# Performance work log

Hardware: AMD Instinct MI355X
Metric: run time of the kernel (lower is better)

Reference implementation:

```python
import jax, jax.numpy as jnp
import numpy as np

D_MODEL = 1024
NUM_HEADS = 8
D_HEAD = D_MODEL // NUM_HEADS
EPS = 1e-5


def layer_norm(x, gamma, beta):
    mu = jnp.mean(x, axis=-1, keepdims=True)
    var = jnp.mean((x - mu) ** 2, axis=-1, keepdims=True)
    return (x - mu) * jax.lax.rsqrt(var + EPS) * gamma + beta


def setup_inputs() -> dict:
    key = jax.random.key(0)
    ks = jax.random.split(key, 16)
    B, N, M, D = 4, 1024, 1024, D_MODEL
    s = 0.02
    inp = {
        "input_states": jax.random.normal(ks[0], (B, N, D), jnp.float32),
        "memory_states": jax.random.normal(ks[1], (B, M, D), jnp.float32),
        "memory_weights": jax.random.uniform(ks[2], (B, M), jnp.float32),
        "memory_masks": jax.random.randint(ks[3], (B, M), 0, 2).astype(bool),
        "attention_factors": jax.random.uniform(ks[4], (B, N, M), jnp.float32),
        "attention_masks": jax.random.randint(ks[5], (B, 1, N, M), 0, 2).astype(bool),
        "Wq": jax.random.normal(ks[6], (D, D), jnp.float32) * s,
        "bq": jnp.zeros((D,), jnp.float32),
        "Wk": jax.random.normal(ks[7], (D, D), jnp.float32) * s,
        "bk": jnp.zeros((D,), jnp.float32),
        "Wv": jax.random.normal(ks[8], (D, D), jnp.float32) * s,
        "bv": jnp.zeros((D,), jnp.float32),
        "Wo": jax.random.normal(ks[9], (D, D), jnp.float32) * s,
        "bo": jnp.zeros((D,), jnp.float32),
        "g1": jnp.ones((D,), jnp.float32),
        "b1": jnp.zeros((D,), jnp.float32),
        "We": jax.random.normal(ks[10], (2 * D, D), jnp.float32) * s,
        "be": jnp.zeros((2 * D,), jnp.float32),
        "Ws": jax.random.normal(ks[11], (D, 2 * D), jnp.float32) * s,
        "bs": jnp.zeros((D,), jnp.float32),
        "g2": jnp.ones((D,), jnp.float32),
        "b2": jnp.zeros((D,), jnp.float32),
    }
    return inp


def reference(input_states, memory_states, memory_weights, memory_masks,
              attention_factors, attention_masks,
              Wq, bq, Wk, bk, Wv, bv, Wo, bo, g1, b1,
              We, be, Ws, bs, g2, b2):
    B, N, D = input_states.shape
    M = memory_states.shape[1]
    H, C = NUM_HEADS, D_HEAD
    # QKV projections, split heads: (B, H, len, C)
    q = (input_states @ Wq.T + bq).reshape(B, N, H, C).transpose(0, 2, 1, 3)
    k = (memory_states @ Wk.T + bk).reshape(B, M, H, C).transpose(0, 2, 1, 3)
    v = (memory_states @ Wv.T + bv).reshape(B, M, H, C).transpose(0, 2, 1, 3)
    scores = jnp.einsum('bhnc,bhmc->bhnm', q, k) / jnp.sqrt(jnp.float32(C))
    scores = attention_factors[:, None, :, :] * scores
    scores = scores * memory_weights[:, None, None, :]
    neg_inf = jnp.float32(-jnp.inf)
    scores = jnp.where(memory_masks[:, None, None, :], neg_inf, scores)
    scores = jnp.where(attention_masks, neg_inf, scores)
    attn = jax.nn.softmax(scores, axis=-1)  # (B,H,N,M)
    hidden = jnp.einsum('bhnm,bhmc->bhnc', attn, v)
    hidden = hidden.transpose(0, 2, 1, 3).reshape(B, N, D)
    hidden = hidden @ Wo.T + bo
    out1 = layer_norm(hidden + input_states, g1, b1)
    # FFN: expand -> ReLU -> squeeze -> residual + LN
    h = jax.nn.relu(out1 @ We.T + be)
    h = h @ Ws.T + bs
    out = layer_norm(out1 + h, g2, b2)
    return out, attn
```

## Files before the change

### kernel.cpp

```cpp
#include <hip/hip_runtime.h>
#include <hip/hip_bf16.h>

typedef __bf16 bf16_t;
typedef __bf16 bf16x4 __attribute__((ext_vector_type(4)));
typedef __bf16 bf16x8 __attribute__((ext_vector_type(8)));
typedef float f32x4 __attribute__((ext_vector_type(4)));

typedef const __attribute__((address_space(1))) void gvoid_t;
typedef __attribute__((address_space(3))) void lvoid_t;

#define MB (1UL<<20)
#define NEGINF (-__builtin_inff())
#define SCALE 0.08838834764831845f

__device__ __forceinline__ void gload_lds16(const void* g, void* l) {
    __builtin_amdgcn_global_load_lds((gvoid_t*)g, (lvoid_t*)l, 16, 0, 0);
}

__global__ __launch_bounds__(256)
void cast8_kernel(const float* __restrict__ s0, bf16_t* __restrict__ d0,
                  const float* __restrict__ s1, bf16_t* __restrict__ d1,
                  const float* __restrict__ s2, bf16_t* __restrict__ d2,
                  const float* __restrict__ s3, bf16_t* __restrict__ d3,
                  const float* __restrict__ s4, bf16_t* __restrict__ d4,
                  const float* __restrict__ s5, bf16_t* __restrict__ d5,
                  const float* __restrict__ s6, bf16_t* __restrict__ d6,
                  const float* __restrict__ s7, bf16_t* __restrict__ d7)
{
    long i = (long)blockIdx.x * 256 + threadIdx.x;
    const float* src; bf16_t* dst; long l;
    if      (i < 262144L)  { src = s0; dst = d0; l = i; }
    else if (i < 524288L)  { src = s1; dst = d1; l = i - 262144L; }
    else if (i < 786432L)  { src = s2; dst = d2; l = i - 524288L; }
    else if (i < 1048576L) { src = s3; dst = d3; l = i - 786432L; }
    else if (i < 1572864L) { src = s4; dst = d4; l = i - 1048576L; }
    else if (i < 2097152L) { src = s5; dst = d5; l = i - 1572864L; }
    else if (i < 3145728L) { src = s6; dst = d6; l = i - 2097152L; }
    else                   { src = s7; dst = d7; l = i - 3145728L; }
    float4 f = ((const float4*)src)[l];
    bf16x4 o;
    o[0] = (bf16_t)f.x; o[1] = (bf16_t)f.y; o[2] = (bf16_t)f.z; o[3] = (bf16_t)f.w;
    ((bf16x4*)dst)[l] = o;
}

template<int TM, int OUT_BF16, int HAS_BIAS, int RELU, int HAS_RES, int VT_OUT>
__global__ __launch_bounds__(256)
void gemm_bt(const bf16_t* __restrict__ Ap, int lda,
             const bf16_t* __restrict__ Bp, int ldb,
             const float* __restrict__ bias,
             const float* __restrict__ res, int ldres,
             void* __restrict__ Cp, int ldc,
             int K, int tilesN,
             long aOffB, long aOffH, long bOffB, long bOffH, long cOffZ, int nH)
{
    __shared__ bf16_t sA[2 * TM * 32];
    __shared__ bf16_t sB[2 * 128 * 32];

    const int z = blockIdx.y;
    const int zb = z / nH, zh = z % nH;
    Ap += zb * aOffB + zh * aOffH;
    Bp += zb * bOffB + zh * bOffH;
    const long cOff = (long)z * cOffZ;

    const int tile = blockIdx.x;
    const int tm = tile / tilesN, tn = tile % tilesN;
    const int rowBase = tm * TM, colBase = tn * 128;
    const int t = threadIdx.x;
    const int wave = t >> 6, lane = t & 63;
    const int wr = (TM == 128) ? ((wave >> 1) * 64) : 0;
    const int wc = (TM == 128) ? ((wave & 1) * 64) : (wave * 32);
    constexpr int NF = (TM == 128) ? 4 : 2;

    f32x4 acc[4][NF] = {};

    const int e0 = t * 8;
    const int srow = e0 >> 5, scol = e0 & 31;

    auto stage = [&](int tt, int bi) {
        const int k0 = tt * 32;
        #pragma unroll
        for (int r = 0; r < TM / 64; ++r) {
            const int row = r * 64 + srow;
            gload_lds16(Ap + (long)(rowBase + row) * lda + k0 + scol,
                        (char*)sA + bi * (TM * 64) + r * 4096 + wave * 1024);
        }
        #pragma unroll
        for (int r = 0; r < 2; ++r) {
            const int row = r * 64 + srow;
            gload_lds16(Bp + (long)(colBase + row) * ldb + k0 + scol,
                        (char*)sB + bi * 8192 + r * 4096 + wave * 1024);
        }
    };

    const int nt = K >> 5;
    stage(0, 0);

    const int kf = (lane >> 4) * 8;
    const int lr = lane & 15;

    for (int tt = 0; tt < nt; ++tt) {
        const int cur = tt & 1;
        if (tt + 1 < nt) {
            stage(tt + 1, cur ^ 1);
            if constexpr (TM == 128) {
                asm volatile("s_waitcnt vmcnt(4)" ::: "memory");
            } else {
                asm volatile("s_waitcnt vmcnt(3)" ::: "memory");
            }
        } else {
            asm volatile("s_waitcnt vmcnt(0)" ::: "memory");
        }
        __builtin_amdgcn_s_barrier();

        bf16x8 af[4], bfr[NF];
        #pragma unroll
        for (int m = 0; m < 4; ++m)
            af[m] = *(const bf16x8*)&sA[cur * (TM * 32) + (wr + m * 16 + lr) * 32 + kf];
        #pragma unroll
        for (int n = 0; n < NF; ++n)
            bfr[n] = *(const bf16x8*)&sB[cur * 4096 + (wc + n * 16 + lr) * 32 + kf];
        #pragma unroll
        for (int m = 0; m < 4; ++m)
            #pragma unroll
            for (int n = 0; n < NF; ++n)
                acc[m][n] = __builtin_amdgcn_mfma_f32_16x16x32_bf16(af[m], bfr[n], acc[m][n], 0, 0, 0);

        __builtin_amdgcn_s_barrier();
    }

    #pragma unroll
    for (int m = 0; m < 4; ++m) {
        #pragma unroll
        for (int r = 0; r < 4; ++r) {
            const int i = rowBase + wr + m * 16 + (lane >> 4) * 4 + r;
            #pragma unroll
            for (int n = 0; n < NF; ++n) {
                const int j = colBase + wc + n * 16 + (lane & 15);
                float v = acc[m][n][r];
                if constexpr (HAS_BIAS) v += bias[j];
                if constexpr (RELU) v = fmaxf(v, 0.0f);
                if constexpr (HAS_RES) v += res[(long)i * ldres + j];
                if constexpr (VT_OUT) {
                    const long o = (((long)(i >> 10) * 8 + (j >> 7)) * 128 + (j & 127)) * 1024 + (i & 1023);
                    ((bf16_t*)Cp)[o] = (bf16_t)v;
                } else if constexpr (OUT_BF16) {
                    ((bf16_t*)Cp)[cOff + (long)i * ldc + j] = (bf16_t)v;
                } else {
                    ((float*)Cp)[cOff + (long)i * ldc + j] = v;
                }
            }
        }
    }
}

__global__ __launch_bounds__(256)
void gate_softmax_kernel(float* __restrict__ Sio,
                         const float* __restrict__ factors,
                         const float* __restrict__ weights,
                         const int* __restrict__ mmask,
                         const int* __restrict__ amask)
{
    const int row = blockIdx.x * 4 + (threadIdx.x >> 6);
    const int lane = threadIdx.x & 63;
    const int n = row & 1023;
    const int b = row >> 13;
    float4* p = (float4*)(Sio + (long)row * 1024);
    const float4* fac = (const float4*)(factors + ((long)b * 1024 + n) * 1024);
    const float4* wt  = (const float4*)(weights + (long)b * 1024);
    const int4*   mm  = (const int4*)(mmask + (long)b * 1024);
    const int4*   am  = (const int4*)(amask + ((long)b * 1024 + n) * 1024);

    float vals[16];
    float mx = NEGINF;
    #pragma unroll
    for (int jj = 0; jj < 4; ++jj) {
        const int v4 = lane + jj * 64;
        float4 sc = p[v4];
        float4 fa = fac[v4];
        float4 w4 = wt[v4];
        int4 m4 = mm[v4];
        int4 a4 = am[v4];
        float4 g;
        g.x = (m4.x | a4.x) ? NEGINF : sc.x * SCALE * fa.x * w4.x;
        g.y = (m4.y | a4.y) ? NEGINF : sc.y * SCALE * fa.y * w4.y;
        g.z = (m4.z | a4.z) ? NEGINF : sc.z * SCALE * fa.z * w4.z;
        g.w = (m4.w | a4.w) ? NEGINF : sc.w * SCALE * fa.w * w4.w;
        vals[jj * 4 + 0] = g.x; vals[jj * 4 + 1] = g.y;
        vals[jj * 4 + 2] = g.z; vals[jj * 4 + 3] = g.w;
        mx = fmaxf(mx, fmaxf(fmaxf(g.x, g.y), fmaxf(g.z, g.w)));
    }
    #pragma unroll
    for (int off = 32; off > 0; off >>= 1) mx = fmaxf(mx, __shfl_xor(mx, off));
    float sum = 0.f;
    #pragma unroll
    for (int q = 0; q < 16; ++q) { float e = __expf(vals[q] - mx); vals[q] = e; sum += e; }
    #pragma unroll
    for (int off = 32; off > 0; off >>= 1) sum += __shfl_xor(sum, off);
    const float inv = 1.0f / sum;
    #pragma unroll
    for (int jj = 0; jj < 4; ++jj) {
        const int v4 = lane + jj * 64;
        float4 o;
        o.x = vals[jj * 4 + 0] * inv; o.y = vals[jj * 4 + 1] * inv;
        o.z = vals[jj * 4 + 2] * inv; o.w = vals[jj * 4 + 3] * inv;
        p[v4] = o;
    }
}

__global__ __launch_bounds__(256)
void pv_kernel(const float* __restrict__ Sprob,
               const bf16_t* __restrict__ Vtb,
               bf16_t* __restrict__ hidb)
{
    __shared__ bf16_t sA[2 * 64 * 32];
    __shared__ bf16_t sB[2 * 128 * 32];

    const int bh = blockIdx.y;
    const int b = bh >> 3, h = bh & 7;
    const int rowBase = blockIdx.x * 64;
    const int t = threadIdx.x;
    const int wave = t >> 6, lane = t & 63;
    const int wc = wave * 32;

    const float* Sp = Sprob + (long)bh * 1048576;
    const bf16_t* Bp = Vtb + (long)bh * 131072;

    const int arow = rowBase + (t >> 2);
    const int acol = (t & 3) * 8;
    const float* Srow = Sp + (long)arow * 1024 + acol;

    f32x4 acc[4][2] = {};

    auto stageB = [&](int tt, int bi) {
        const int k0 = tt * 32;
        #pragma unroll
        for (int r = 0; r < 2; ++r) {
            const int row = r * 64 + ((t * 8) >> 5);
            gload_lds16(Bp + (long)row * 1024 + k0 + ((t * 8) & 31),
                        (char*)sB + bi * 8192 + r * 4096 + wave * 1024);
        }
    };

    auto procA = [&](int tt, int bi, float4 s0, float4 s1) {
        bf16x8 pb;
        pb[0] = (bf16_t)s0.x; pb[1] = (bf16_t)s0.y; pb[2] = (bf16_t)s0.z; pb[3] = (bf16_t)s0.w;
        pb[4] = (bf16_t)s1.x; pb[5] = (bf16_t)s1.y; pb[6] = (bf16_t)s1.z; pb[7] = (bf16_t)s1.w;
        *(bf16x8*)((char*)sA + bi * 4096 + t * 16) = pb;
    };

    stageB(0, 0);
    {
        float4 s0 = *(const float4*)Srow;
        float4 s1 = *(const float4*)(Srow + 4);
        procA(0, 0, s0, s1);
    }
    asm volatile("s_waitcnt vmcnt(0)" ::: "memory");
    __syncthreads();

    const int kf = (lane >> 4) * 8;
    const int lr = lane & 15;

    for (int tt = 0; tt < 32; ++tt) {
        const int cur = tt & 1;
        float4 s0, s1;
        if (tt < 31) {
            stageB(tt + 1, cur ^ 1);
            s0 = *(const float4*)(Srow + (tt + 1) * 32);
            s1 = *(const float4*)(Srow + (tt + 1) * 32 + 4);
        }

        bf16x8 af[4], bfr[2];
        #pragma unroll
        for (int m = 0; m < 4; ++m)
            af[m] = *(const bf16x8*)&sA[cur * 2048 + (m * 16 + lr) * 32 + kf];
        #pragma unroll
        for (int n = 0; n < 2; ++n)
            bfr[n] = *(const bf16x8*)&sB[cur * 4096 + (wc + n * 16 + lr) * 32 + kf];
        #pragma unroll
        for (int m = 0; m < 4; ++m)
            #pragma unroll
            for (int n = 0; n < 2; ++n)
                acc[m][n] = __builtin_amdgcn_mfma_f32_16x16x32_bf16(af[m], bfr[n], acc[m][n], 0, 0, 0);

        if (tt < 31) procA(tt + 1, cur ^ 1, s0, s1);

        asm volatile("s_waitcnt vmcnt(0)" ::: "memory");
        __syncthreads();
    }

    #pragma unroll
    for (int m = 0; m < 4; ++m) {
        #pragma unroll
        for (int r = 0; r < 4; ++r) {
            const int i = rowBase + m * 16 + (lane >> 4) * 4 + r;
            #pragma unroll
            for (int n = 0; n < 2; ++n) {
                const int j = wc + n * 16 + (lane & 15);
                hidb[((long)b * 1024 + i) * 1024 + h * 128 + j] = (bf16_t)acc[m][n][r];
            }
        }
    }
}

template<int WRITE_BF16>
__global__ __launch_bounds__(256)
void ln_kernel(const float* __restrict__ x,
               const float* __restrict__ g,
               const float* __restrict__ bt,
               float* __restrict__ outf,
               bf16_t* __restrict__ outb)
{
    const int row = blockIdx.x * 4 + (threadIdx.x >> 6);
    const int lane = threadIdx.x & 63;
    const float* p = x + (long)row * 1024;
    float v[16];
    float s = 0.f;
    #pragma unroll
    for (int jj = 0; jj < 4; ++jj) {
        float4 f = ((const float4*)p)[lane + jj * 64];
        v[jj * 4 + 0] = f.x; v[jj * 4 + 1] = f.y; v[jj * 4 + 2] = f.z; v[jj * 4 + 3] = f.w;
        s += f.x + f.y + f.z + f.w;
    }
    #pragma unroll
    for (int off = 32; off > 0; off >>= 1) s += __shfl_xor(s, off);
    const float mu = s * (1.0f / 1024.0f);
    float q = 0.f;
    #pragma unroll
    for (int i = 0; i < 16; ++i) { float d = v[i] - mu; q += d * d; }
    #pragma unroll
    for (int off = 32; off > 0; off >>= 1) q += __shfl_xor(q, off);
    const float rstd = rsqrtf(q * (1.0f / 1024.0f) + 1e-5f);
    #pragma unroll
    for (int jj = 0; jj < 4; ++jj) {
        const int v4 = lane + jj * 64;
        float4 gg = ((const float4*)g)[v4];
        float4 bb = ((const float4*)bt)[v4];
        float4 o;
        o.x = (v[jj * 4 + 0] - mu) * rstd * gg.x + bb.x;
        o.y = (v[jj * 4 + 1] - mu) * rstd * gg.y + bb.y;
        o.z = (v[jj * 4 + 2] - mu) * rstd * gg.z + bb.z;
        o.w = (v[jj * 4 + 3] - mu) * rstd * gg.w + bb.w;
        ((float4*)outf)[(long)row * 256 + v4] = o;
        if constexpr (WRITE_BF16) {
            bf16x4 ob;
            ob[0] = (bf16_t)o.x; ob[1] = (bf16_t)o.y; ob[2] = (bf16_t)o.z; ob[3] = (bf16_t)o.w;
            ((bf16x4*)outb)[(long)row * 256 + v4] = ob;
        }
    }
}

extern "C" void kernel_launch(void* const* d_in, const int* in_sizes, int n_in,
                              void* d_out, int out_size, void* d_ws, size_t ws_size,
                              hipStream_t stream)
{
    (void)in_sizes; (void)n_in; (void)out_size; (void)ws_size;
    const float* input_states     = (const float*)d_in[0];
    const float* memory_states    = (const float*)d_in[1];
    const float* memory_weights   = (const float*)d_in[2];
    const int*   memory_masks     = (const int*)d_in[3];
    const float* attention_factors= (const float*)d_in[4];
    const int*   attention_masks  = (const int*)d_in[5];
    const float* Wq = (const float*)d_in[6];
    const float* bq = (const float*)d_in[7];
    const float* Wk = (const float*)d_in[8];
    const float* bk = (const float*)d_in[9];
    const float* Wv = (const float*)d_in[10];
    const float* bv = (const float*)d_in[11];
    const float* Wo = (const float*)d_in[12];
    const float* bo = (const float*)d_in[13];
    const float* g1 = (const float*)d_in[14];
    const float* b1 = (const float*)d_in[15];
    const float* We = (const float*)d_in[16];
    const float* be = (const float*)d_in[17];
    const float* Ws = (const float*)d_in[18];
    const float* bs = (const float*)d_in[19];
    const float* g2 = (const float*)d_in[20];
    const float* b2 = (const float*)d_in[21];

    float* out0 = (float*)d_out;
    float* attn = (float*)d_out + 4L * 1024 * 1024;

    char* ws = (char*)d_ws;
    bf16_t* Wqb  = (bf16_t*)(ws + 0 * MB);
    bf16_t* Wkb  = (bf16_t*)(ws + 2 * MB);
    bf16_t* Wvb  = (bf16_t*)(ws + 4 * MB);
    bf16_t* Wob  = (bf16_t*)(ws + 6 * MB);
    bf16_t* Web  = (bf16_t*)(ws + 8 * MB);
    bf16_t* Wsb  = (bf16_t*)(ws + 12 * MB);
    bf16_t* inb  = (bf16_t*)(ws + 16 * MB);
    bf16_t* memb = (bf16_t*)(ws + 24 * MB);
    bf16_t* Qb   = (bf16_t*)(ws + 32 * MB);
    bf16_t* Kb   = (bf16_t*)(ws + 40 * MB);
    bf16_t* Vtb  = (bf16_t*)(ws + 48 * MB);
    bf16_t* hidb = (bf16_t*)(ws + 56 * MB);
    float*  preLN= (float*)(ws + 64 * MB);
    float*  out1f= (float*)(ws + 80 * MB);
    bf16_t* out1b= (bf16_t*)(ws + 96 * MB);
    bf16_t* hffn = (bf16_t*)(ws + 104 * MB);

    cast8_kernel<<<16384, 256, 0, stream>>>(Wq, Wqb, Wk, Wkb, Wv, Wvb, Wo, Wob,
                                            We, Web, Ws, Wsb,
                                            input_states, inb, memory_states, memb);

    gemm_bt<64,1,1,0,0,0><<<dim3(512, 1), 256, 0, stream>>>(
        inb, 1024, Wqb, 1024, bq, nullptr, 0, Qb, 1024, 1024, 8, 0,0,0,0,0, 1);
    gemm_bt<64,1,1,0,0,0><<<dim3(512, 1), 256, 0, stream>>>(
        memb, 1024, Wkb, 1024, bk, nullptr, 0, Kb, 1024, 1024, 8, 0,0,0,0,0, 1);
    gemm_bt<64,1,1,0,0,1><<<dim3(512, 1), 256, 0, stream>>>(
        memb, 1024, Wvb, 1024, bv, nullptr, 0, Vtb, 1024, 1024, 8, 0,0,0,0,0, 1);
    gemm_bt<128,0,0,0,0,0><<<dim3(64, 32), 256, 0, stream>>>(
        Qb, 1024, Kb, 1024, nullptr, nullptr, 0, attn, 1024, 128, 8,
        1048576L, 128L, 1048576L, 128L, 1048576L, 8);
    gate_softmax_kernel<<<8192, 256, 0, stream>>>(attn, attention_factors,
                                                  memory_weights, memory_masks,
                                                  attention_masks);
    pv_kernel<<<dim3(16, 32), 256, 0, stream>>>(attn, Vtb, hidb);
    gemm_bt<64,0,1,0,1,0><<<dim3(512, 1), 256, 0, stream>>>(
        hidb, 1024, Wob, 1024, bo, input_states, 1024, preLN, 1024, 1024, 8, 0,0,0,0,0, 1);
    ln_kernel<1><<<1024, 256, 0, stream>>>(preLN, g1, b1, out1f, out1b);
    gemm_bt<128,1,1,1,0,0><<<dim3(512, 1), 256, 0, stream>>>(
        out1b, 1024, Web, 1024, be, nullptr, 0, hffn, 2048, 1024, 16, 0,0,0,0,0, 1);
    gemm_bt<64,0,1,0,1,0><<<dim3(512, 1), 256, 0, stream>>>(
        hffn, 2048, Wsb, 2048, bs, out1f, 1024, preLN, 1024, 2048, 8, 0,0,0,0,0, 1);
    ln_kernel<0><<<1024, 256, 0, stream>>>(preLN, g2, b2, out0, nullptr);
}
```

Before: 333.0 us.

## Fuse Q/K/V projections into one launch and add XCD tile swizzle

Replaces three separate projection GEMM launches with a single qkv_gemm kernel that uses blockIdx.y to pick the operation. That kernel overlaps the next-stage loads with compute through a partial vmcnt wait and raw barriers. An XCD-aware tile remap is also added to the generic GEMM and the new kernel, so neighbouring tiles land on the same die and share L2. The aim is to cut launch overhead and tail underutilisation and to improve cache locality. The tradeoff is extra code duplication and reliance on hand-placed waitcnt and barrier correctness.

After: 318.0 us. 4.5% less time.

```diff
diff --git a/kernel.cpp b/kernel.cpp
--- a/kernel.cpp
+++ b/kernel.cpp
@@ -15,6 +15,11 @@
 
 __device__ __forceinline__ void gload_lds16(const void* g, void* l) {
     __builtin_amdgcn_global_load_lds((gvoid_t*)g, (lvoid_t*)l, 16, 0, 0);
+}
+
+__device__ __forceinline__ int xcd_swizzle(int tile, int nwg) {
+    const int cpx = nwg >> 3;
+    return (tile & 7) * cpx + (tile >> 3);
 }
 
 __global__ __launch_bounds__(256)
@@ -62,7 +67,7 @@
     Bp += zb * bOffB + zh * bOffH;
     const long cOff = (long)z * cOffZ;
 
-    const int tile = blockIdx.x;
+    const int tile = xcd_swizzle(blockIdx.x, gridDim.x);
     const int tm = tile / tilesN, tn = tile % tilesN;
     const int rowBase = tm * TM, colBase = tn * 128;
     const int t = threadIdx.x;
@@ -154,6 +159,99 @@
 }
 
 __global__ __launch_bounds__(256)
+void qkv_gemm(const bf16_t* __restrict__ inb, const bf16_t* __restrict__ memb,
+              const bf16_t* __restrict__ Wqb, const bf16_t* __restrict__ Wkb,
+              const bf16_t* __restrict__ Wvb,
+              const float* __restrict__ bq, const float* __restrict__ bk,
+              const float* __restrict__ bv,
+              bf16_t* __restrict__ Qb, bf16_t* __restrict__ Kb,
+              bf16_t* __restrict__ Vtb)
+{
+    __shared__ bf16_t sA[2 * 64 * 32];
+    __shared__ bf16_t sB[2 * 128 * 32];
+
+    const int op = blockIdx.y;
+    const bf16_t* Ap = (op == 0) ? inb : memb;
+    const bf16_t* Bp = (op == 0) ? Wqb : (op == 1) ? Wkb : Wvb;
+    const float* bias = (op == 0) ? bq : (op == 1) ? bk : bv;
+
+    const int tile = xcd_swizzle(blockIdx.x, gridDim.x);
+    const int tm = tile >> 3, tn = tile & 7;
+    const int rowBase = tm * 64, colBase = tn * 128;
+    const int t = threadIdx.x;
+    const int wave = t >> 6, lane = t & 63;
+    const int wc = wave * 32;
+
+    f32x4 acc[4][2] = {};
+
+    const int e0 = t * 8;
+    const int srow = e0 >> 5, scol = e0 & 31;
+
+    auto stage = [&](int tt, int bi) {
+        const int k0 = tt * 32;
+        gload_lds16(Ap + (long)(rowBase + srow) * 1024 + k0 + scol,
+                    (char*)sA + bi * 4096 + wave * 1024);
+        #pragma unroll
+        for (int r = 0; r < 2; ++r) {
+            const int row = r * 64 + srow;
+            gload_lds16(Bp + (long)(colBase + row) * 1024 + k0 + scol,
+                        (char*)sB + bi * 8192 + r * 4096 + wave * 1024);
+        }
+    };
+
+    stage(0, 0);
+
+    const int kf = (lane >> 4) * 8;
+    const int lr = lane & 15;
+
+    for (int tt = 0; tt < 32; ++tt) {
+        const int cur = tt & 1;
+        if (tt + 1 < 32) {
+            stage(tt + 1, cur ^ 1);
+            asm volatile("s_waitcnt vmcnt(3)" ::: "memory");
+        } else {
+            asm volatile("s_waitcnt vmcnt(0)" ::: "memory");
+        }
+        __builtin_amdgcn_s_barrier();
+
+        bf16x8 af[4], bfr[2];
+        #pragma unroll
+        for (int m = 0; m < 4; ++m)
+            af[m] = *(const bf16x8*)&sA[cur * 2048 + (m * 16 + lr) * 32 + kf];
+        #pragma unroll
+        for (int n = 0; n < 2; ++n)
+            bfr[n] = *(const bf16x8*)&sB[cur * 4096 + (wc + n * 16 + lr) * 32 + kf];
+        #pragma unroll
+        for (int m = 0; m < 4; ++m)
+            #pragma unroll
+            for (int n = 0; n < 2; ++n)
+                acc[m][n] = __builtin_amdgcn_mfma_f32_16x16x32_bf16(af[m], bfr[n], acc[m][n], 0, 0, 0);
+
+        __builtin_amdgcn_s_barrier();
+    }
+
+    bf16_t* Cp = (op == 0) ? Qb : (op == 1) ? Kb : Vtb;
+    #pragma unroll
+    for (int m = 0; m < 4; ++m) {
+        #pragma unroll
+        for (int r = 0; r < 4; ++r) {
+            const int i = rowBase + m * 16 + (lane >> 4) * 4 + r;
+            #pragma unroll
+            for (int n = 0; n < 2; ++n) {
+                const int j = colBase + wc + n * 16 + (lane & 15);
+                float v = acc[m][n][r] + bias[j];
+                if (op == 2) {
+                    const long o = (((long)(i >> 10) * 8 + (j >> 7)) * 128 + (j & 127)) * 1024 + (i & 1023);
+                    Cp[o] = (bf16_t)v;
+                } else {
+                    Cp[(long)i * 1024 + j] = (bf16_t)v;
+                }
+            }
+        }
+    }
+}
+
+__global__ __launch_bounds__(256)
 void gate_softmax_kernel(float* __restrict__ Sio,
                          const float* __restrict__ factors,
                          const float* __restrict__ weights,
@@ -241,7 +339,7 @@
         }
     };
 
-    auto procA = [&](int tt, int bi, float4 s0, float4 s1) {
+    auto procA = [&](int bi, float4 s0, float4 s1) {
         bf16x8 pb;
         pb[0] = (bf16_t)s0.x; pb[1] = (bf16_t)s0.y; pb[2] = (bf16_t)s0.z; pb[3] = (bf16_t)s0.w;
         pb[4] = (bf16_t)s1.x; pb[5] = (bf16_t)s1.y; pb[6] = (bf16_t)s1.z; pb[7] = (bf16_t)s1.w;
@@ -252,7 +350,7 @@
     {
         float4 s0 = *(const float4*)Srow;
         float4 s1 = *(const float4*)(Srow + 4);
-        procA(0, 0, s0, s1);
+        procA(0, s0, s1);
     }
     asm volatile("s_waitcnt vmcnt(0)" ::: "memory");
     __syncthreads();
@@ -282,7 +380,7 @@
             for (int n = 0; n < 2; ++n)
                 acc[m][n] = __builtin_amdgcn_mfma_f32_16x16x32_bf16(af[m], bfr[n], acc[m][n], 0, 0, 0);
 
-        if (tt < 31) procA(tt + 1, cur ^ 1, s0, s1);
+        if (tt < 31) procA(cur ^ 1, s0, s1);
 
         asm volatile("s_waitcnt vmcnt(0)" ::: "memory");
         __syncthreads();
@@ -402,12 +500,8 @@
                                             We, Web, Ws, Wsb,
                                             input_states, inb, memory_states, memb);
 
-    gemm_bt<64,1,1,0,0,0><<<dim3(512, 1), 256, 0, stream>>>(
-        inb, 1024, Wqb, 1024, bq, nullptr, 0, Qb, 1024, 1024, 8, 0,0,0,0,0, 1);
-    gemm_bt<64,1,1,0,0,0><<<dim3(512, 1), 256, 0, stream>>>(
-        memb, 1024, Wkb, 1024, bk, nullptr, 0, Kb, 1024, 1024, 8, 0,0,0,0,0, 1);
-    gemm_bt<64,1,1,0,0,1><<<dim3(512, 1), 256, 0, stream>>>(
-        memb, 1024, Wvb, 1024, bv, nullptr, 0, Vtb, 1024, 1024, 8, 0,0,0,0,0, 1);
+    qkv_gemm<<<dim3(512, 3), 256, 0, stream>>>(inb, memb, Wqb, Wkb, Wvb,
+                                               bq, bk, bv, Qb, Kb, Vtb);
     gemm_bt<128,0,0,0,0,0><<<dim3(64, 32), 256, 0, stream>>>(
         Qb, 1024, Kb, 1024, nullptr, nullptr, 0, attn, 1024, 128, 8,
         1048576L, 128L, 1048576L, 128L, 1048576L, 8);
```
